# Optimization experiments

Measured on AMD Instinct MI355X. Metric: run time of the kernel, lower is better.

## Reference

```python
import jax, jax.numpy as jnp
import numpy as np

NEG_SLOPE = 0.2
EPS = 1e-6


def setup_inputs() -> dict:
    key = jax.random.key(0)
    k1, k2 = jax.random.split(key)
    B, C, N = 4, 64, 32768
    x = jax.random.normal(k1, (B, C, 3, N), dtype=jnp.float32)
    # VNLinear weight: nn.Linear(in, out, bias=False).weight -> [out, in]
    W = jax.random.normal(k2, (C, C), dtype=jnp.float32) * (1.0 / np.sqrt(C))
    return {"x": x, "W": W}


def reference(x, W):
    # VNLinear: kron(W, eye(3)) conv2d == per-3-vector channel mix
    # d[b,o,v,n] = sum_i W[o,i] * x[b,i,v,n]
    d = jnp.einsum('oi,bivn->bovn', W, x)
    dotprod = jnp.sum(x * d, axis=2, keepdims=True)      # [B,C,1,N]
    d_norm_sq = jnp.sum(d * d, axis=2, keepdims=True)    # [B,C,1,N]
    neg = x - (1.0 - NEG_SLOPE) * (dotprod / (d_norm_sq + EPS)) * d
    return jnp.where(dotprod >= 0, x, neg)
```

## Files before the change

kernel.cpp:

```cpp
#include <hip/hip_runtime.h>

#define NEG_SLOPE 0.2f
#define EPS 1e-6f


#define C_CH 64
#define V_DIM 3
#define N_FULL 32768
#define NT 32
#define THREADS 256
#define TPB 4

typedef __attribute__((ext_vector_type(8))) short bf16x8;
typedef __attribute__((ext_vector_type(4))) float f32x4;

__device__ __forceinline__ ushort f2bf(float f) {
    union { float f; unsigned u; } v; v.f = f;
    unsigned r = v.u + 0x7FFFu + ((v.u >> 16) & 1u);
    return (ushort)(r >> 16);
}
__device__ __forceinline__ float bf2f(ushort s) {
    union { unsigned u; float f; } v; v.u = ((unsigned)s) << 16; return v.f;
}
__device__ __forceinline__ unsigned pack_hl(float x) {
    union { float f; unsigned u; } a; a.f = x;
    unsigned t0 = a.u + 0x8000u;
    union { unsigned u; float f; } hb; hb.u = t0 & 0xffff0000u;
    union { float f; unsigned u; } rb; rb.f = x - hb.f;
    return __builtin_amdgcn_perm(t0, rb.u, 0x07060302u);
}
__device__ __forceinline__ float u2f(unsigned u) {
    union { unsigned u; float f; } v; v.u = u; return v.f;
}

__device__ __forceinline__ int swz(int row) { return ((row >> 3) & 1) << 4; }

__global__ __launch_bounds__(THREADS, 3)
void vn_pipe(const float* __restrict__ x,
             const float* __restrict__ Wf,
             float* __restrict__ out) {
    __shared__ unsigned xs[2][V_DIM * C_CH][NT];

    const int t     = threadIdx.x;
    const int tile0 = blockIdx.x * TPB;
    const int b     = tile0 >> 10;
    const float* xbase = x   + (size_t)b * (C_CH * V_DIM * N_FULL);
    float*       obase = out + (size_t)b * (C_CH * V_DIM * N_FULL);

    const int lane = t & 63;
    const int w    = t >> 6;
    const int wo   = w >> 1;
    const int wn   = w & 1;
    const int l4   = lane & 15;
    const int hi   = lane >> 4;


    float4 xr[6];
    {
        const float* xb = xbase + ((tile0 & 1023) << 5);
        #pragma unroll
        for (int it = 0; it < 6; ++it) {
            int idx = t + it * THREADS;
            xr[it] = *(const float4*)(xb + (size_t)(idx >> 3) * N_FULL + ((idx & 7) << 2));
        }
    }

    bf16x8 Ah[2][2], Al[2][2];
    #pragma unroll
    for (int m = 0; m < 2; ++m)
        #pragma unroll
        for (int kh = 0; kh < 2; ++kh) {
            const float* wp = Wf + (size_t)(wo * 32 + m * 16 + l4) * C_CH + kh * 32 + hi * 8;
            float4 wa = *(const float4*)wp;
            float4 wb = *(const float4*)(wp + 4);
            float wf[8] = {wa.x, wa.y, wa.z, wa.w, wb.x, wb.y, wb.z, wb.w};
            bf16x8 h, l;
            #pragma unroll
            for (int j = 0; j < 8; ++j) {
                ushort hb = f2bf(wf[j]);
                h[j] = (short)hb;
                l[j] = (short)f2bf(wf[j] - bf2f(hb));
            }
            Ah[m][kh] = h; Al[m][kh] = l;
        }

    #pragma unroll
    for (int it = 0; it < 6; ++it) {
        int idx = t + it * THREADS;
        int r   = idx >> 3;
        int c4  = (idx & 7) << 2;
        int i   = (r * 171) >> 9;
        int v   = r - 3 * i;
        int rowp = v * 64 + i;
        unsigned p[4] = {pack_hl(xr[it].x), pack_hl(xr[it].y),
                         pack_hl(xr[it].z), pack_hl(xr[it].w)};
        *(uint4*)&xs[0][rowp][c4 ^ swz(rowp)] = *(const uint4*)p;
    }
    __syncthreads();

    const int acol = (wn * 16 + l4) ^ ((hi & 1) << 4);
    const int n    = wn * 16 + l4;
    const int ecol = n ^ ((hi >> 1) << 4);

    #pragma unroll
    for (int tt = 0; tt < TPB; ++tt) {
        const int cur = tt & 1;
        const int n0c = ((tile0 + tt) & 1023) << 5;

        if (tt + 1 < TPB) {
            const float* xb = xbase + (((tile0 + tt + 1) & 1023) << 5);
            #pragma unroll
            for (int it = 0; it < 6; ++it) {
                int idx = t + it * THREADS;
                xr[it] = *(const float4*)(xb + (size_t)(idx >> 3) * N_FULL + ((idx & 7) << 2));
            }
        }

        f32x4 acc[2][3];
        #pragma unroll
        for (int m = 0; m < 2; ++m)
            #pragma unroll
            for (int v = 0; v < 3; ++v)
                acc[m][v] = (f32x4){0.f, 0.f, 0.f, 0.f};

        #pragma unroll
        for (int v = 0; v < 3; ++v) {
            #pragma unroll
            for (int kh = 0; kh < 2; ++kh) {
                const int rowb = v * 64 + kh * 32 + hi * 8;
                unsigned p[8];
                #pragma unroll
                for (int j = 0; j < 8; ++j)
                    p[j] = xs[cur][rowb + j][acol];
                union { bf16x8 v8; unsigned d[4]; } BH, BL;
                #pragma unroll
                for (int q = 0; q < 4; ++q) {
                    BH.d[q] = __builtin_amdgcn_perm(p[2 * q + 1], p[2 * q], 0x07060302u);
                    BL.d[q] = __builtin_amdgcn_perm(p[2 * q + 1], p[2 * q], 0x05040100u);
                }
                #pragma unroll
                for (int m = 0; m < 2; ++m) {
                    acc[m][v] = __builtin_amdgcn_mfma_f32_16x16x32_bf16(Ah[m][kh], BH.v8, acc[m][v], 0, 0, 0);
                    acc[m][v] = __builtin_amdgcn_mfma_f32_16x16x32_bf16(Ah[m][kh], BL.v8, acc[m][v], 0, 0, 0);
                    acc[m][v] = __builtin_amdgcn_mfma_f32_16x16x32_bf16(Al[m][kh], BH.v8, acc[m][v], 0, 0, 0);
                }
            }
        }

        float* ob = obase + n0c + n;
        #pragma unroll
        for (int m = 0; m < 2; ++m) {
            #pragma unroll
            for (int rr = 0; rr < 4; ++rr) {
                const int o = wo * 32 + m * 16 + hi * 4 + rr;
                float xv[3], dv[3];
                #pragma unroll
                for (int v = 0; v < 3; ++v) {
                    unsigned p = xs[cur][v * 64 + o][ecol];
                    xv[v] = u2f(p & 0xffff0000u) + u2f(p << 16);
                    dv[v] = acc[m][v][rr];
                }
                float dot  = xv[0] * dv[0] + xv[1] * dv[1] + xv[2] * dv[2];
                float dnsq = dv[0] * dv[0] + dv[1] * dv[1] + dv[2] * dv[2];
                float f = (1.0f - NEG_SLOPE) * dot * __builtin_amdgcn_rcpf(dnsq + EPS);
                f = (dot >= 0.f) ? 0.f : f;
                float o0 = fmaf(-f, dv[0], xv[0]);
                float o1 = fmaf(-f, dv[1], xv[1]);
                float o2 = fmaf(-f, dv[2], xv[2]);
                float* op = ob + (size_t)o * (V_DIM * N_FULL);
                op[0 * N_FULL] = o0;
                op[1 * N_FULL] = o1;
                op[2 * N_FULL] = o2;
            }
        }

        if (tt + 1 < TPB) {
            #pragma unroll
            for (int it = 0; it < 6; ++it) {
                int idx = t + it * THREADS;
                int r   = idx >> 3;
                int c4  = (idx & 7) << 2;
                int i   = (r * 171) >> 9;
                int v   = r - 3 * i;
                int rowp = v * 64 + i;
                unsigned p[4] = {pack_hl(xr[it].x), pack_hl(xr[it].y),
                                 pack_hl(xr[it].z), pack_hl(xr[it].w)};
                *(uint4*)&xs[cur ^ 1][rowp][c4 ^ swz(rowp)] = *(const uint4*)p;
            }
        }
        __syncthreads();
    }
}

extern "C" void kernel_launch(void* const* d_in, const int* in_sizes, int n_in,
                              void* d_out, int out_size, void* d_ws, size_t ws_size,
                              hipStream_t stream) {
    const float* x = (const float*)d_in[0];
    const float* W = (const float*)d_in[1];
    float* out = (float*)d_out;

    const int B = 4;
    const int blocks = B * (N_FULL / NT) / TPB;
    vn_pipe<<<blocks, THREADS, 0, stream>>>(x, W, out);
}
```

Baseline: 38.69 us.

## Double block size so each wave computes one 16-row output slice

```diff
diff --git a/kernel.cpp b/kernel.cpp
--- a/kernel.cpp
+++ b/kernel.cpp
@@ -8,7 +8,7 @@
 #define V_DIM 3
 #define N_FULL 32768
 #define NT 32
-#define THREADS 256
+#define THREADS 512
 #define TPB 4
 
 typedef __attribute__((ext_vector_type(8))) short bf16x8;
@@ -35,7 +35,7 @@
 
 __device__ __forceinline__ int swz(int row) { return ((row >> 3) & 1) << 4; }
 
-__global__ __launch_bounds__(THREADS, 3)
+__global__ __launch_bounds__(THREADS, 6)
 void vn_pipe(const float* __restrict__ x,
              const float* __restrict__ Wf,
              float* __restrict__ out) {
@@ -55,37 +55,35 @@
     const int hi   = lane >> 4;
 
 
-    float4 xr[6];
+    float4 xr[3];
     {
         const float* xb = xbase + ((tile0 & 1023) << 5);
         #pragma unroll
-        for (int it = 0; it < 6; ++it) {
+        for (int it = 0; it < 3; ++it) {
             int idx = t + it * THREADS;
             xr[it] = *(const float4*)(xb + (size_t)(idx >> 3) * N_FULL + ((idx & 7) << 2));
         }
     }
 
-    bf16x8 Ah[2][2], Al[2][2];
+    bf16x8 Ah[2], Al[2];
     #pragma unroll
-    for (int m = 0; m < 2; ++m)
+    for (int kh = 0; kh < 2; ++kh) {
+        const float* wp = Wf + (size_t)(wo * 16 + l4) * C_CH + kh * 32 + hi * 8;
+        float4 wa = *(const float4*)wp;
+        float4 wb = *(const float4*)(wp + 4);
+        float wf[8] = {wa.x, wa.y, wa.z, wa.w, wb.x, wb.y, wb.z, wb.w};
+        bf16x8 h, l;
         #pragma unroll
-        for (int kh = 0; kh < 2; ++kh) {
-            const float* wp = Wf + (size_t)(wo * 32 + m * 16 + l4) * C_CH + kh * 32 + hi * 8;
-            float4 wa = *(const float4*)wp;
-            float4 wb = *(const float4*)(wp + 4);
-            float wf[8] = {wa.x, wa.y, wa.z, wa.w, wb.x, wb.y, wb.z, wb.w};
-            bf16x8 h, l;
-            #pragma unroll
-            for (int j = 0; j < 8; ++j) {
-                ushort hb = f2bf(wf[j]);
-                h[j] = (short)hb;
-                l[j] = (short)f2bf(wf[j] - bf2f(hb));
-            }
-            Ah[m][kh] = h; Al[m][kh] = l;
+        for (int j = 0; j < 8; ++j) {
+            ushort hb = f2bf(wf[j]);
+            h[j] = (short)hb;
+            l[j] = (short)f2bf(wf[j] - bf2f(hb));
         }
+        Ah[kh] = h; Al[kh] = l;
+    }
 
     #pragma unroll
-    for (int it = 0; it < 6; ++it) {
+    for (int it = 0; it < 3; ++it) {
         int idx = t + it * THREADS;
         int r   = idx >> 3;
         int c4  = (idx & 7) << 2;
@@ -110,18 +108,16 @@
         if (tt + 1 < TPB) {
             const float* xb = xbase + (((tile0 + tt + 1) & 1023) << 5);
             #pragma unroll
-            for (int it = 0; it < 6; ++it) {
+            for (int it = 0; it < 3; ++it) {
                 int idx = t + it * THREADS;
                 xr[it] = *(const float4*)(xb + (size_t)(idx >> 3) * N_FULL + ((idx & 7) << 2));
             }
         }
 
-        f32x4 acc[2][3];
+        f32x4 acc[3];
         #pragma unroll
-        for (int m = 0; m < 2; ++m)
-            #pragma unroll
-            for (int v = 0; v < 3; ++v)
-                acc[m][v] = (f32x4){0.f, 0.f, 0.f, 0.f};
+        for (int v = 0; v < 3; ++v)
+            acc[v] = (f32x4){0.f, 0.f, 0.f, 0.f};
 
         #pragma unroll
         for (int v = 0; v < 3; ++v) {
@@ -138,45 +134,39 @@
                     BH.d[q] = __builtin_amdgcn_perm(p[2 * q + 1], p[2 * q], 0x07060302u);
                     BL.d[q] = __builtin_amdgcn_perm(p[2 * q + 1], p[2 * q], 0x05040100u);
                 }
-                #pragma unroll
-                for (int m = 0; m < 2; ++m) {
-                    acc[m][v] = __builtin_amdgcn_mfma_f32_16x16x32_bf16(Ah[m][kh], BH.v8, acc[m][v], 0, 0, 0);
-                    acc[m][v] = __builtin_amdgcn_mfma_f32_16x16x32_bf16(Ah[m][kh], BL.v8, acc[m][v], 0, 0, 0);
-                    acc[m][v] = __builtin_amdgcn_mfma_f32_16x16x32_bf16(Al[m][kh], BH.v8, acc[m][v], 0, 0, 0);
-                }
+                acc[v] = __builtin_amdgcn_mfma_f32_16x16x32_bf16(Ah[kh], BH.v8, acc[v], 0, 0, 0);
+                acc[v] = __builtin_amdgcn_mfma_f32_16x16x32_bf16(Ah[kh], BL.v8, acc[v], 0, 0, 0);
+                acc[v] = __builtin_amdgcn_mfma_f32_16x16x32_bf16(Al[kh], BH.v8, acc[v], 0, 0, 0);
             }
         }
 
         float* ob = obase + n0c + n;
         #pragma unroll
-        for (int m = 0; m < 2; ++m) {
+        for (int rr = 0; rr < 4; ++rr) {
+            const int o = wo * 16 + hi * 4 + rr;
+            float xv[3], dv[3];
             #pragma unroll
-            for (int rr = 0; rr < 4; ++rr) {
-                const int o = wo * 32 + m * 16 + hi * 4 + rr;
-                float xv[3], dv[3];
-                #pragma unroll
-                for (int v = 0; v < 3; ++v) {
-                    unsigned p = xs[cur][v * 64 + o][ecol];
-                    xv[v] = u2f(p & 0xffff0000u) + u2f(p << 16);
-                    dv[v] = acc[m][v][rr];
-                }
-                float dot  = xv[0] * dv[0] + xv[1] * dv[1] + xv[2] * dv[2];
-                float dnsq = dv[0] * dv[0] + dv[1] * dv[1] + dv[2] * dv[2];
-                float f = (1.0f - NEG_SLOPE) * dot * __builtin_amdgcn_rcpf(dnsq + EPS);
-                f = (dot >= 0.f) ? 0.f : f;
-                float o0 = fmaf(-f, dv[0], xv[0]);
-                float o1 = fmaf(-f, dv[1], xv[1]);
-                float o2 = fmaf(-f, dv[2], xv[2]);
-                float* op = ob + (size_t)o * (V_DIM * N_FULL);
-                op[0 * N_FULL] = o0;
-                op[1 * N_FULL] = o1;
-                op[2 * N_FULL] = o2;
+            for (int v = 0; v < 3; ++v) {
+                unsigned p = xs[cur][v * 64 + o][ecol];
+                xv[v] = u2f(p & 0xffff0000u) + u2f(p << 16);
+                dv[v] = acc[v][rr];
             }
+            float dot  = xv[0] * dv[0] + xv[1] * dv[1] + xv[2] * dv[2];
+            float dnsq = dv[0] * dv[0] + dv[1] * dv[1] + dv[2] * dv[2];
+            float f = (1.0f - NEG_SLOPE) * dot * __builtin_amdgcn_rcpf(dnsq + EPS);
+            f = (dot >= 0.f) ? 0.f : f;
+            float o0 = fmaf(-f, dv[0], xv[0]);
+            float o1 = fmaf(-f, dv[1], xv[1]);
+            float o2 = fmaf(-f, dv[2], xv[2]);
+            float* op = ob + (size_t)o * (V_DIM * N_FULL);
+            op[0 * N_FULL] = o0;
+            op[1 * N_FULL] = o1;
+            op[2 * N_FULL] = o2;
         }
 
         if (tt + 1 < TPB) {
             #pragma unroll
-            for (int it = 0; it < 6; ++it) {
+            for (int it = 0; it < 3; ++it) {
                 int idx = t + it * THREADS;
                 int r   = idx >> 3;
                 int c4  = (idx & 7) << 2;
```

After: 53.70 us. 1.39x slower.
